# Performance work log

Hardware: AMD Instinct MI355X
Metric: run time of the kernel (lower is better)

## Reference

```python
import jax, jax.numpy as jnp
import numpy as np

NU, NI, D, C, V, E, L = 100000, 50000, 128, 5, 200000, 200000, 10


def setup_inputs() -> dict:
    key = jax.random.key(0)
    ks = jax.random.split(key, 16)
    s = lambda fan_in: 1.0 / np.sqrt(fan_in)
    return {
        "urf": jax.random.normal(ks[0], (NU, D), jnp.float32),
        "irf": jax.random.normal(ks[1], (NI, D), jnp.float32),
        "utf": jax.random.normal(ks[2], (NU, D), jnp.float32),
        "itf": jax.random.normal(ks[3], (NI, D), jnp.float32),
        "w1r": jax.random.normal(ks[4], (2 * D, D), jnp.float32) * s(2 * D),
        "w2r": jax.random.normal(ks[5], (D, D), jnp.float32) * s(D),
        "w1t": jax.random.normal(ks[6], (2 * D, D), jnp.float32) * s(2 * D),
        "w2t": jax.random.normal(ks[7], (D, D), jnp.float32) * s(D),
        "wp": jax.random.normal(ks[8], (D, C), jnp.float32) * s(D),
        "emb": jax.random.normal(ks[9], (V, D), jnp.float32),
        "src": jax.random.randint(ks[10], (E,), 0, NU, jnp.int32),
        "dst": jax.random.randint(ks[11], (E,), 0, NI, jnp.int32),
        "sentence_id": jax.random.randint(ks[12], (E, L), 0, V, jnp.int32),
        "neg_sid": jax.random.randint(ks[13], (E, L), 1, V, jnp.int32),
    }


def _review_feature(emb, sid):
    # masked mean-pool of sentence embeddings: [E, L] -> [E, D]
    length = (sid > 0).astype(jnp.float32).sum(axis=-1, keepdims=True) + 1e-9
    return emb[sid].sum(axis=-2) / length


def reference(urf, irf, utf, itf, w1r, w2r, w1t, w2t, wp, emb,
              src, dst, sentence_id, neg_sid):
    # edge-wise gather of src (user) / dst (item) features + concat  [E, 2D]
    rf = jnp.concatenate([urf[src], irf[dst]], axis=1)
    rh = jax.nn.relu(rf @ w1r) @ w2r                      # rating_linear  [E, D]
    pr = rh @ wp                                          # rating_predictor [E, C]
    tf = jnp.concatenate([utf[src], itf[dst]], axis=1)
    th = jax.nn.relu(tf @ w1t) @ w2t + rh                 # topic_linear + residual
    pos_review = _review_feature(emb, sentence_id)        # [E, D]
    neg_review = _review_feature(emb, neg_sid)            # [E, D]
    pos_score = (th * pos_review).sum(axis=1)             # [E]
    neg_score = (th * neg_review).sum(axis=1)
    loss = -jax.nn.log_sigmoid(pos_score - neg_score)     # -log(sigmoid(pos-neg))
    return pr, loss.mean(), loss.mean()
```

## Files before the change

### kernel.cpp

```cpp
#include <hip/hip_runtime.h>

#define NU_ 100000
#define NI_ 50000
#define D_  128
#define C_  5
#define V_  200000
#define E_  200000
#define L_  10

typedef __bf16 bf16x8 __attribute__((ext_vector_type(8)));
typedef unsigned short u16;
typedef u16 u16x8 __attribute__((ext_vector_type(8)));
typedef float f32x4 __attribute__((ext_vector_type(4)));

#define W1R_OFF 0
#define W2R_OFF 32768
#define W1T_OFF 49152
#define W2T_OFF 81920
#define WTOT    98304
#define EMB_BYTE_OFF (256 * 1024)
#define EMB_ELEMS    (V_ * D_)
#define TH_BYTE_OFF  (EMB_BYTE_OFF + EMB_ELEMS * 2)
#define TH_BYTES     ((size_t)E_ * D_ * 2)

__device__ __forceinline__ u16 f2bf(float x) {
    union { float f; unsigned int u; } v; v.f = x;
    unsigned int u = v.u;
    return (u16)((u + 0x7FFFu + ((u >> 16) & 1u)) >> 16);
}
__device__ __forceinline__ float bfhi(unsigned int u) {
    union { unsigned int u; float f; } v; v.u = u & 0xFFFF0000u; return v.f;
}
__device__ __forceinline__ float bflo(unsigned int u) {
    union { unsigned int u; float f; } v; v.u = u << 16; return v.f;
}

__global__ void prep_kernel(const float* __restrict__ w1r, const float* __restrict__ w2r,
                            const float* __restrict__ w1t, const float* __restrict__ w2t,
                            u16* __restrict__ wbuf, float* __restrict__ loss_acc) {
    int idx = blockIdx.x * blockDim.x + threadIdx.x;
    if (idx == 0) *loss_acc = 0.f;
    if (idx >= WTOT) return;
    const float* src; int base;
    if (idx < W2R_OFF)      { src = w1r; base = W1R_OFF; }
    else if (idx < W1T_OFF) { src = w2r; base = W2R_OFF; }
    else if (idx < W2T_OFF) { src = w1t; base = W1T_OFF; }
    else                    { src = w2t; base = W2T_OFF; }
    int local = idx - base;
    int j = local & 7;
    int g = local >> 3;
    int n = g & 127;
    int kq = g >> 7;
    wbuf[idx] = f2bf(src[(kq * 8 + j) * 128 + n]);
}

__global__ void cvt_kernel(const float* __restrict__ src, u16* __restrict__ dst, int n8) {
    int i = blockIdx.x * blockDim.x + threadIdx.x;
    if (i >= n8) return;
    float4 a = *(const float4*)(src + (size_t)i * 8);
    float4 b = *(const float4*)(src + (size_t)i * 8 + 4);
    u16x8 v;
    v[0] = f2bf(a.x); v[1] = f2bf(a.y); v[2] = f2bf(a.z); v[3] = f2bf(a.w);
    v[4] = f2bf(b.x); v[5] = f2bf(b.y); v[6] = f2bf(b.z); v[7] = f2bf(b.w);
    *(u16x8*)(dst + (size_t)i * 8) = v;
}

__device__ __forceinline__ void stage_half(const float* __restrict__ row, int lane, u16* buf) {
    int m = lane >> 2, q = lane & 3;
    const float* seg = row + q * 32;
#pragma unroll
    for (int i = 0; i < 4; i++) {
        float4 a = *(const float4*)(seg + i * 8);
        float4 b = *(const float4*)(seg + i * 8 + 4);
        u16x8 v;
        v[0] = f2bf(a.x); v[1] = f2bf(a.y); v[2] = f2bf(a.z); v[3] = f2bf(a.w);
        v[4] = f2bf(b.x); v[5] = f2bf(b.y); v[6] = f2bf(b.z); v[7] = f2bf(b.w);
        *(u16x8*)(buf + ((q * 4 + i) * 16 + m) * 8) = v;
    }
}

template <int KT>
__device__ __forceinline__ void gemm_tile(const u16* aLDS, const u16* __restrict__ Wg,
                                          int lq, int ln, f32x4 acc[8]) {
#pragma unroll
    for (int kt = 0; kt < KT; kt++) {
        bf16x8 af = *(const bf16x8*)(aLDS + ((kt * 4 + lq) * 16 + ln) * 8);
#pragma unroll
        for (int nt = 0; nt < 8; nt++) {
            bf16x8 bfv = *(const bf16x8*)(Wg + (size_t)((kt * 4 + lq) * 128 + nt * 16 + ln) * 8);
            acc[nt] = __builtin_amdgcn_mfma_f32_16x16x32_bf16(af, bfv, acc[nt], 0, 0, 0);
        }
    }
}

__device__ __forceinline__ void store_h_relu(const f32x4 acc[8], u16* buf, int lq, int ln) {
#pragma unroll
    for (int nt = 0; nt < 8; nt++)
#pragma unroll
        for (int reg = 0; reg < 4; reg++) {
            float h = fmaxf(acc[nt][reg], 0.f);
            int dcol = nt * 16 + ln;
            int r = lq * 4 + reg;
            buf[((dcol >> 3) * 16 + r) * 8 + (dcol & 7)] = f2bf(h);
        }
}

__device__ __forceinline__ void mlp(const float* __restrict__ uF, const float* __restrict__ iF,
                                    const int* __restrict__ srcI, const int* __restrict__ dstI,
                                    int ebase, int lane, int lq, int ln,
                                    const u16* __restrict__ w1, const u16* __restrict__ w2,
                                    u16* bufA, u16* bufB, f32x4 acc[8]) {
    int e = ebase + (lane >> 2);
    int su = srcI[e], sd = dstI[e];
    f32x4 h1[8];
#pragma unroll
    for (int nt = 0; nt < 8; nt++) h1[nt] = (f32x4){0.f, 0.f, 0.f, 0.f};

    stage_half(uF + (size_t)su * D_, lane, bufA);
    __syncthreads();
    gemm_tile<4>(bufA, w1, lq, ln, h1);
    __syncthreads();
    stage_half(iF + (size_t)sd * D_, lane, bufA);
    __syncthreads();
    gemm_tile<4>(bufA, w1 + 16384, lq, ln, h1);
    store_h_relu(h1, bufB, lq, ln);
    __syncthreads();
    gemm_tile<4>(bufB, w2, lq, ln, acc);
}

__device__ __forceinline__ float softplus_(float x) {
    return fmaxf(x, 0.f) + log1pf(expf(-fabsf(x)));
}


__global__ __launch_bounds__(256, 3) void mlp_kernel(
    const float* __restrict__ urf, const float* __restrict__ irf,
    const float* __restrict__ utf, const float* __restrict__ itf,
    const float* __restrict__ wp,
    const int* __restrict__ srcI, const int* __restrict__ dstI,
    const u16* __restrict__ wbuf, float* __restrict__ out,
    u16* __restrict__ thB) {
    __shared__ u16 smem[4 * 4096];
    const int tid = threadIdx.x;
    const int w = tid >> 6;
    const int lane = tid & 63;
    const int lq = lane >> 4;
    const int ln = lane & 15;
    u16* bufA = smem + w * 4096;
    u16* bufB = bufA + 2048;
    const int ebase = blockIdx.x * 64 + w * 16;

    f32x4 rh[8];
#pragma unroll
    for (int nt = 0; nt < 8; nt++) rh[nt] = (f32x4){0.f, 0.f, 0.f, 0.f};
    mlp(urf, irf, srcI, dstI, ebase, lane, lq, ln,
        wbuf + W1R_OFF, wbuf + W2R_OFF, bufA, bufB, rh);

    {
        float pp[4][5];
#pragma unroll
        for (int r = 0; r < 4; r++)
#pragma unroll
            for (int c = 0; c < 5; c++) pp[r][c] = 0.f;
#pragma unroll
        for (int nt = 0; nt < 8; nt++) {
            int d = nt * 16 + ln;
            float wpc[5];
#pragma unroll
            for (int c = 0; c < 5; c++) wpc[c] = wp[d * 5 + c];
#pragma unroll
            for (int reg = 0; reg < 4; reg++)
#pragma unroll
                for (int c = 0; c < 5; c++) pp[reg][c] += rh[nt][reg] * wpc[c];
        }
#pragma unroll
        for (int off = 1; off < 16; off <<= 1)
#pragma unroll
            for (int reg = 0; reg < 4; reg++)
#pragma unroll
                for (int c = 0; c < 5; c++)
                    pp[reg][c] += __shfl_xor(pp[reg][c], off, 64);
        if (ln == 0) {
#pragma unroll
            for (int reg = 0; reg < 4; reg++) {
                int e = ebase + lq * 4 + reg;
#pragma unroll
                for (int c = 0; c < 5; c++) out[(size_t)e * 5 + c] = pp[reg][c];
            }
        }
    }

    __syncthreads();
    f32x4 th[8];
#pragma unroll
    for (int nt = 0; nt < 8; nt++) th[nt] = rh[nt];
    mlp(utf, itf, srcI, dstI, ebase, lane, lq, ln,
        wbuf + W1T_OFF, wbuf + W2T_OFF, bufA, bufB, th);

    __syncthreads();
    float* thb = (float*)bufA;
#pragma unroll
    for (int nt = 0; nt < 8; nt++)
#pragma unroll
        for (int reg = 0; reg < 4; reg++)
            thb[(lq * 4 + reg) * 128 + nt * 16 + ln] = th[nt][reg];
    __syncthreads();

#pragma unroll
    for (int m = 0; m < 16; m++) {
        float2 ab = *(const float2*)(thb + m * 128 + lane * 2);
        unsigned pk = (unsigned)f2bf(ab.x) | ((unsigned)f2bf(ab.y) << 16);
        ((unsigned*)(thB + (size_t)(ebase + m) * D_))[lane] = pk;
    }
}

__global__ __launch_bounds__(256, 8) void review_kernel(
    const u16* __restrict__ thB, const u16* __restrict__ embB,
    const int* __restrict__ sidI, const int* __restrict__ nsidI,
    float* __restrict__ loss_acc) {
    __shared__ float red[4];
    const int tid = threadIdx.x;
    const int lane = tid & 63;
    const int gl = tid & 15;
    const int e = blockIdx.x * 16 + (tid >> 4);

    int ip = 0, in_ = 0;
    if (gl < L_) { ip = sidI[e * L_ + gl]; in_ = nsidI[e * L_ + gl]; }

    float th8[8];
    {
        union { u16x8 v; unsigned int u[4]; } tu;
        tu.v = *(const u16x8*)(thB + (size_t)e * D_ + gl * 8);
#pragma unroll
        for (int k = 0; k < 4; k++) {
            th8[2 * k]     = bflo(tu.u[k]);
            th8[2 * k + 1] = bfhi(tu.u[k]);
        }
    }

    float ps = 0.f, ns = 0.f;
    float pc = (gl < L_ && ip > 0) ? 1.f : 0.f;
    float nc = (gl < L_ && in_ > 0) ? 1.f : 0.f;

#pragma unroll
    for (int i = 0; i < L_; i++) {
        int s = __shfl(ip, i, 16);
        union { u16x8 v; unsigned int u[4]; } cv;
        cv.v = *(const u16x8*)(embB + (size_t)s * D_ + gl * 8);
        int t = __shfl(in_, i, 16);
        union { u16x8 v; unsigned int u[4]; } nv;
        nv.v = *(const u16x8*)(embB + (size_t)t * D_ + gl * 8);
#pragma unroll
        for (int k = 0; k < 4; k++) {
            ps = fmaf(th8[2 * k],     bflo(cv.u[k]), ps);
            ps = fmaf(th8[2 * k + 1], bfhi(cv.u[k]), ps);
        }
#pragma unroll
        for (int k = 0; k < 4; k++) {
            ns = fmaf(th8[2 * k],     bflo(nv.u[k]), ns);
            ns = fmaf(th8[2 * k + 1], bfhi(nv.u[k]), ns);
        }
    }

#pragma unroll
    for (int off = 1; off < 16; off <<= 1) {
        ps += __shfl_xor(ps, off, 64);
        ns += __shfl_xor(ns, off, 64);
        pc += __shfl_xor(pc, off, 64);
        nc += __shfl_xor(nc, off, 64);
    }
    float val = softplus_(ns / (nc + 1e-9f) - ps / (pc + 1e-9f));
    float wl = (gl == 0) ? val : 0.f;
    wl += __shfl_xor(wl, 16, 64);
    wl += __shfl_xor(wl, 32, 64);
    if (lane == 0) red[tid >> 6] = wl;
    __syncthreads();
    if (tid == 0) atomicAdd(loss_acc, red[0] + red[1] + red[2] + red[3]);
}

template <bool EB>
__global__ __launch_bounds__(256, 3) void fused_kernel(
    const float* __restrict__ urf, const float* __restrict__ irf,
    const float* __restrict__ utf, const float* __restrict__ itf,
    const float* __restrict__ wp, const float* __restrict__ emb,
    const u16* __restrict__ embB,
    const int* __restrict__ srcI, const int* __restrict__ dstI,
    const int* __restrict__ sidI, const int* __restrict__ nsidI,
    const u16* __restrict__ wbuf, float* __restrict__ loss_acc,
    float* __restrict__ out) {
    __shared__ u16 smem[4 * 4096];
    const int tid = threadIdx.x;
    const int w = tid >> 6;
    const int lane = tid & 63;
    const int lq = lane >> 4;
    const int ln = lane & 15;
    u16* bufA = smem + w * 4096;
    u16* bufB = bufA + 2048;
    const int ebase = blockIdx.x * 64 + w * 16;

    f32x4 rh[8];
#pragma unroll
    for (int nt = 0; nt < 8; nt++) rh[nt] = (f32x4){0.f, 0.f, 0.f, 0.f};
    mlp(urf, irf, srcI, dstI, ebase, lane, lq, ln,
        wbuf + W1R_OFF, wbuf + W2R_OFF, bufA, bufB, rh);

    {
        float pp[4][5];
#pragma unroll
        for (int r = 0; r < 4; r++)
#pragma unroll
            for (int c = 0; c < 5; c++) pp[r][c] = 0.f;
#pragma unroll
        for (int nt = 0; nt < 8; nt++) {
            int d = nt * 16 + ln;
            float wpc[5];
#pragma unroll
            for (int c = 0; c < 5; c++) wpc[c] = wp[d * 5 + c];
#pragma unroll
            for (int reg = 0; reg < 4; reg++)
#pragma unroll
                for (int c = 0; c < 5; c++) pp[reg][c] += rh[nt][reg] * wpc[c];
        }
#pragma unroll
        for (int off = 1; off < 16; off <<= 1)
#pragma unroll
            for (int reg = 0; reg < 4; reg++)
#pragma unroll
                for (int c = 0; c < 5; c++)
                    pp[reg][c] += __shfl_xor(pp[reg][c], off, 64);
        if (ln == 0) {
#pragma unroll
            for (int reg = 0; reg < 4; reg++) {
                int e = ebase + lq * 4 + reg;
#pragma unroll
                for (int c = 0; c < 5; c++) out[(size_t)e * 5 + c] = pp[reg][c];
            }
        }
    }

    __syncthreads();
    f32x4 th[8];
#pragma unroll
    for (int nt = 0; nt < 8; nt++) th[nt] = rh[nt];
    mlp(utf, itf, srcI, dstI, ebase, lane, lq, ln,
        wbuf + W1T_OFF, wbuf + W2T_OFF, bufA, bufB, th);

    __syncthreads();
    float* thb = (float*)bufA;
    if constexpr (EB) {
#pragma unroll
        for (int nt = 0; nt < 8; nt++)
#pragma unroll
            for (int reg = 0; reg < 4; reg++) {
                int col = nt * 16 + ln;
                thb[((lq * 4 + reg) * 16 + (col >> 3)) * 8 + (col & 7)] = th[nt][reg];
            }
    } else {
#pragma unroll
        for (int nt = 0; nt < 8; nt++)
#pragma unroll
            for (int reg = 0; reg < 4; reg++)
                thb[(lq * 4 + reg) * 128 + nt * 16 + ln] = th[nt][reg];
    }
    __syncthreads();

    float wave_loss = 0.f;
    if constexpr (EB) {
        const int g = lane >> 4, gl = lane & 15;
        for (int it = 0; it < 4; it++) {
            int m = it * 4 + g;
            int e = ebase + m;
            float th8[8];
            *(f32x4*)th8       = *(const f32x4*)(thb + (m * 16 + gl) * 8);
            *(f32x4*)(th8 + 4) = *(const f32x4*)(thb + (m * 16 + gl) * 8 + 4);
            float ps = 0.f, ns = 0.f;
            int pcnt = 0, ncnt = 0;
#pragma unroll
            for (int i = 0; i < L_; i++) {
                int s = sidI[e * L_ + i];
                pcnt += (s > 0) ? 1 : 0;
                union { u16x8 v; unsigned int u[4]; } cv;
                cv.v = *(const u16x8*)(embB + (size_t)s * D_ + gl * 8);
#pragma unroll
                for (int k = 0; k < 4; k++) {
                    ps = fmaf(th8[2 * k],     bflo(cv.u[k]), ps);
                    ps = fmaf(th8[2 * k + 1], bfhi(cv.u[k]), ps);
                }
            }
#pragma unroll
            for (int i = 0; i < L_; i++) {
                int s = nsidI[e * L_ + i];
                ncnt += (s > 0) ? 1 : 0;
                union { u16x8 v; unsigned int u[4]; } cv;
                cv.v = *(const u16x8*)(embB + (size_t)s * D_ + gl * 8);
#pragma unroll
                for (int k = 0; k < 4; k++) {
                    ns = fmaf(th8[2 * k],     bflo(cv.u[k]), ns);
                    ns = fmaf(th8[2 * k + 1], bfhi(cv.u[k]), ns);
                }
            }
#pragma unroll
            for (int off = 1; off < 16; off <<= 1) {
                ps += __shfl_xor(ps, off, 64);
                ns += __shfl_xor(ns, off, 64);
            }
            if (gl == 0) {
                ps /= ((float)pcnt + 1e-9f);
                ns /= ((float)ncnt + 1e-9f);
                wave_loss += softplus_(ns - ps);
            }
        }
        wave_loss += __shfl_xor(wave_loss, 16, 64);
        wave_loss += __shfl_xor(wave_loss, 32, 64);
    } else {
        const int h = lane >> 5, hl = lane & 31;
        for (int mp = 0; mp < 16; mp += 2) {
            int m = mp + h;
            int e = ebase + m;
            float4 t4 = *(const float4*)(thb + m * 128 + hl * 4);
            float ps = 0.f, ns = 0.f;
            int pcnt = 0, ncnt = 0;
#pragma unroll
            for (int i = 0; i < L_; i++) {
                int s = sidI[e * L_ + i];
                pcnt += (s > 0) ? 1 : 0;
                float4 ev = *(const float4*)(emb + (size_t)s * D_ + hl * 4);
                ps += t4.x * ev.x + t4.y * ev.y + t4.z * ev.z + t4.w * ev.w;
            }
#pragma unroll
            for (int i = 0; i < L_; i++) {
                int s = nsidI[e * L_ + i];
                ncnt += (s > 0) ? 1 : 0;
                float4 ev = *(const float4*)(emb + (size_t)s * D_ + hl * 4);
                ns += t4.x * ev.x + t4.y * ev.y + t4.z * ev.z + t4.w * ev.w;
            }
#pragma unroll
            for (int off = 1; off < 32; off <<= 1) {
                ps += __shfl_xor(ps, off, 64);
                ns += __shfl_xor(ns, off, 64);
            }
            if (hl == 0) {
                ps /= ((float)pcnt + 1e-9f);
                ns /= ((float)ncnt + 1e-9f);
                wave_loss += softplus_(ns - ps);
            }
        }
        wave_loss += __shfl_xor(wave_loss, 32, 64);
    }
    if (lane == 0) atomicAdd(loss_acc, wave_loss);
}

__global__ void finish_kernel(const float* __restrict__ loss_acc, float* __restrict__ out) {
    float v = loss_acc[0] * (1.0f / (float)E_);
    out[(size_t)E_ * C_]     = v;
    out[(size_t)E_ * C_ + 1] = v;
}

extern "C" void kernel_launch(void* const* d_in, const int* in_sizes, int n_in,
                              void* d_out, int out_size, void* d_ws, size_t ws_size,
                              hipStream_t stream) {
    const float* urf = (const float*)d_in[0];
    const float* irf = (const float*)d_in[1];
    const float* utf = (const float*)d_in[2];
    const float* itf = (const float*)d_in[3];
    const float* w1r = (const float*)d_in[4];
    const float* w2r = (const float*)d_in[5];
    const float* w1t = (const float*)d_in[6];
    const float* w2t = (const float*)d_in[7];
    const float* wp  = (const float*)d_in[8];
    const float* emb = (const float*)d_in[9];
    const int* srcI  = (const int*)d_in[10];
    const int* dstI  = (const int*)d_in[11];
    const int* sidI  = (const int*)d_in[12];
    const int* nsidI = (const int*)d_in[13];
    float* out = (float*)d_out;

    float* loss_acc = (float*)d_ws;
    u16* wbuf = (u16*)((char*)d_ws + 256);
    u16* embB = (u16*)((char*)d_ws + EMB_BYTE_OFF);
    u16* thB  = (u16*)((char*)d_ws + TH_BYTE_OFF);

    bool eb = ws_size >= (size_t)EMB_BYTE_OFF + (size_t)EMB_ELEMS * 2;
    bool tb = ws_size >= (size_t)TH_BYTE_OFF + TH_BYTES;

    prep_kernel<<<(WTOT + 255) / 256, 256, 0, stream>>>(w1r, w2r, w1t, w2t, wbuf, loss_acc);
    if (eb)
        cvt_kernel<<<(EMB_ELEMS / 8 + 255) / 256, 256, 0, stream>>>(emb, embB, EMB_ELEMS / 8);

    if (tb) {
        mlp_kernel<<<E_ / 64, 256, 0, stream>>>(
            urf, irf, utf, itf, wp, srcI, dstI, wbuf, out, thB);
        review_kernel<<<E_ / 16, 256, 0, stream>>>(
            thB, embB, sidI, nsidI, loss_acc);
    } else if (eb) {
        fused_kernel<true><<<E_ / 64, 256, 0, stream>>>(
            urf, irf, utf, itf, wp, emb, embB,
            srcI, dstI, sidI, nsidI, wbuf, loss_acc, out);
    } else {
        fused_kernel<false><<<E_ / 64, 256, 0, stream>>>(
            urf, irf, utf, itf, wp, emb, embB,
            srcI, dstI, sidI, nsidI, wbuf, loss_acc, out);
    }

    finish_kernel<<<1, 1, 0, stream>>>(loss_acc, out);
}
```

Measured before the change: 611.6 us.

## Quantize embedding table to FP8 and replace block barriers with per-wave LDS fences

The embedding table is now converted to an e4m3-style FP8 copy instead of bf16, which halves the bytes gathered in the review kernel and the bytes written by the conversion pass. The decode uses a shift-and-scale trick rather than hardware conversion. The MLP stages both the user and item halves into separate LDS buffers before the GEMMs, and replaces __syncthreads with wave-local lgkmcnt waits, since each wave owns its own LDS region. Costs: more LDS per block, larger quantization error in the review scores that may break tolerance, and the bf16-embedding fused fallback path is removed.

```diff
diff --git a/kernel.cpp b/kernel.cpp
--- a/kernel.cpp
+++ b/kernel.cpp
@@ -20,7 +20,7 @@
 #define WTOT    98304
 #define EMB_BYTE_OFF (256 * 1024)
 #define EMB_ELEMS    (V_ * D_)
-#define TH_BYTE_OFF  (EMB_BYTE_OFF + EMB_ELEMS * 2)
+#define TH_BYTE_OFF  (EMB_BYTE_OFF + EMB_ELEMS)
 #define TH_BYTES     ((size_t)E_ * D_ * 2)
 
 __device__ __forceinline__ u16 f2bf(float x) {
@@ -33,6 +33,29 @@
 }
 __device__ __forceinline__ float bflo(unsigned int u) {
     union { unsigned int u; float f; } v; v.u = u << 16; return v.f;
+}
+
+__device__ __forceinline__ unsigned f2fp8(float x) {
+    union { float f; unsigned u; } v; v.f = x;
+    unsigned s = (v.u >> 24) & 0x80u;
+    float ax = fabsf(x);
+    if (ax < 0.0078125f) return s;
+    if (ax < 0.015625f)  return s | 0x08u;
+    if (ax > 448.f)      return s | 0x7Eu;
+    unsigned u = v.u & 0x7FFFFFFFu;
+    unsigned r = u + 0x7FFFFu + ((u >> 20) & 1u);
+    unsigned c = (r >> 20) - 960u;
+    if (c > 0x7Eu) c = 0x7Eu;
+    return s | c;
+}
+__device__ __forceinline__ float fp8dec(unsigned b) {
+    unsigned t = ((b & 0x80u) << 24) | ((b & 0x7Fu) << 20);
+    union { unsigned u; float f; } v; v.u = t;
+    return v.f * 0x1.0p+120f;
+}
+
+__device__ __forceinline__ void lds_fence() {
+    asm volatile("s_waitcnt lgkmcnt(0)" ::: "memory");
 }
 
 __global__ void prep_kernel(const float* __restrict__ w1r, const float* __restrict__ w2r,
@@ -54,15 +77,15 @@
     wbuf[idx] = f2bf(src[(kq * 8 + j) * 128 + n]);
 }
 
-__global__ void cvt_kernel(const float* __restrict__ src, u16* __restrict__ dst, int n8) {
+__global__ void cvt8_kernel(const float* __restrict__ src, unsigned char* __restrict__ dst, int n8) {
     int i = blockIdx.x * blockDim.x + threadIdx.x;
     if (i >= n8) return;
     float4 a = *(const float4*)(src + (size_t)i * 8);
     float4 b = *(const float4*)(src + (size_t)i * 8 + 4);
-    u16x8 v;
-    v[0] = f2bf(a.x); v[1] = f2bf(a.y); v[2] = f2bf(a.z); v[3] = f2bf(a.w);
-    v[4] = f2bf(b.x); v[5] = f2bf(b.y); v[6] = f2bf(b.z); v[7] = f2bf(b.w);
-    *(u16x8*)(dst + (size_t)i * 8) = v;
+    uint2 v;
+    v.x = f2fp8(a.x) | (f2fp8(a.y) << 8) | (f2fp8(a.z) << 16) | (f2fp8(a.w) << 24);
+    v.y = f2fp8(b.x) | (f2fp8(b.y) << 8) | (f2fp8(b.z) << 16) | (f2fp8(b.w) << 24);
+    *(uint2*)(dst + (size_t)i * 8) = v;
 }
 
 __device__ __forceinline__ void stage_half(const float* __restrict__ row, int lane, u16* buf) {
@@ -105,26 +128,20 @@
         }
 }
 
-__device__ __forceinline__ void mlp(const float* __restrict__ uF, const float* __restrict__ iF,
-                                    const int* __restrict__ srcI, const int* __restrict__ dstI,
-                                    int ebase, int lane, int lq, int ln,
-                                    const u16* __restrict__ w1, const u16* __restrict__ w2,
-                                    u16* bufA, u16* bufB, f32x4 acc[8]) {
-    int e = ebase + (lane >> 2);
-    int su = srcI[e], sd = dstI[e];
+__device__ __forceinline__ void mlp2(const float* __restrict__ uRow, const float* __restrict__ iRow,
+                                     int lane, int lq, int ln,
+                                     const u16* __restrict__ w1, const u16* __restrict__ w2,
+                                     u16* bufA, u16* bufC, u16* bufB, f32x4 acc[8]) {
     f32x4 h1[8];
 #pragma unroll
     for (int nt = 0; nt < 8; nt++) h1[nt] = (f32x4){0.f, 0.f, 0.f, 0.f};
-
-    stage_half(uF + (size_t)su * D_, lane, bufA);
-    __syncthreads();
+    stage_half(uRow, lane, bufA);
+    stage_half(iRow, lane, bufC);
+    lds_fence();
     gemm_tile<4>(bufA, w1, lq, ln, h1);
-    __syncthreads();
-    stage_half(iF + (size_t)sd * D_, lane, bufA);
-    __syncthreads();
-    gemm_tile<4>(bufA, w1 + 16384, lq, ln, h1);
+    gemm_tile<4>(bufC, w1 + 16384, lq, ln, h1);
     store_h_relu(h1, bufB, lq, ln);
-    __syncthreads();
+    lds_fence();
     gemm_tile<4>(bufB, w2, lq, ln, acc);
 }
 
@@ -140,21 +157,25 @@
     const int* __restrict__ srcI, const int* __restrict__ dstI,
     const u16* __restrict__ wbuf, float* __restrict__ out,
     u16* __restrict__ thB) {
-    __shared__ u16 smem[4 * 4096];
+    __shared__ u16 smem[4 * 6144];
     const int tid = threadIdx.x;
     const int w = tid >> 6;
     const int lane = tid & 63;
     const int lq = lane >> 4;
     const int ln = lane & 15;
-    u16* bufA = smem + w * 4096;
-    u16* bufB = bufA + 2048;
+    u16* bufA = smem + w * 6144;
+    u16* bufC = bufA + 2048;
+    u16* bufB = bufA + 4096;
     const int ebase = blockIdx.x * 64 + w * 16;
 
+    const int e0 = ebase + (lane >> 2);
+    const int su = srcI[e0], sd = dstI[e0];
+
     f32x4 rh[8];
 #pragma unroll
     for (int nt = 0; nt < 8; nt++) rh[nt] = (f32x4){0.f, 0.f, 0.f, 0.f};
-    mlp(urf, irf, srcI, dstI, ebase, lane, lq, ln,
-        wbuf + W1R_OFF, wbuf + W2R_OFF, bufA, bufB, rh);
+    mlp2(urf + (size_t)su * D_, irf + (size_t)sd * D_, lane, lq, ln,
+         wbuf + W1R_OFF, wbuf + W2R_OFF, bufA, bufC, bufB, rh);
 
     {
         float pp[4][5];
@@ -190,21 +211,19 @@
         }
     }
 
-    __syncthreads();
     f32x4 th[8];
 #pragma unroll
     for (int nt = 0; nt < 8; nt++) th[nt] = rh[nt];
-    mlp(utf, itf, srcI, dstI, ebase, lane, lq, ln,
-        wbuf + W1T_OFF, wbuf + W2T_OFF, bufA, bufB, th);
-
-    __syncthreads();
+    mlp2(utf + (size_t)su * D_, itf + (size_t)sd * D_, lane, lq, ln,
+         wbuf + W1T_OFF, wbuf + W2T_OFF, bufA, bufC, bufB, th);
+
     float* thb = (float*)bufA;
 #pragma unroll
     for (int nt = 0; nt < 8; nt++)
 #pragma unroll
         for (int reg = 0; reg < 4; reg++)
             thb[(lq * 4 + reg) * 128 + nt * 16 + ln] = th[nt][reg];
-    __syncthreads();
+    lds_fence();
 
 #pragma unroll
     for (int m = 0; m < 16; m++) {
@@ -215,7 +234,7 @@
 }
 
 __global__ __launch_bounds__(256, 8) void review_kernel(
-    const u16* __restrict__ thB, const u16* __restrict__ embB,
+    const u16* __restrict__ thB, const unsigned char* __restrict__ embF8,
     const int* __restrict__ sidI, const int* __restrict__ nsidI,
     float* __restrict__ loss_acc) {
     __shared__ float red[4];
@@ -245,20 +264,18 @@
 #pragma unroll
     for (int i = 0; i < L_; i++) {
         int s = __shfl(ip, i, 16);
-        union { u16x8 v; unsigned int u[4]; } cv;
-        cv.v = *(const u16x8*)(embB + (size_t)s * D_ + gl * 8);
+        uint2 cv = *(const uint2*)(embF8 + (size_t)s * D_ + gl * 8);
         int t = __shfl(in_, i, 16);
-        union { u16x8 v; unsigned int u[4]; } nv;
-        nv.v = *(const u16x8*)(embB + (size_t)t * D_ + gl * 8);
-#pragma unroll
-        for (int k = 0; k < 4; k++) {
-            ps = fmaf(th8[2 * k],     bflo(cv.u[k]), ps);
-            ps = fmaf(th8[2 * k + 1], bfhi(cv.u[k]), ps);
-        }
-#pragma unroll
-        for (int k = 0; k < 4; k++) {
-            ns = fmaf(th8[2 * k],     bflo(nv.u[k]), ns);
-            ns = fmaf(th8[2 * k + 1], bfhi(nv.u[k]), ns);
+        uint2 nv = *(const uint2*)(embF8 + (size_t)t * D_ + gl * 8);
+#pragma unroll
+        for (int j = 0; j < 4; j++) {
+            ps = fmaf(th8[j],     fp8dec((cv.x >> (8 * j)) & 0xFFu), ps);
+            ps = fmaf(th8[4 + j], fp8dec((cv.y >> (8 * j)) & 0xFFu), ps);
+        }
+#pragma unroll
+        for (int j = 0; j < 4; j++) {
+            ns = fmaf(th8[j],     fp8dec((nv.x >> (8 * j)) & 0xFFu), ns);
+            ns = fmaf(th8[4 + j], fp8dec((nv.y >> (8 * j)) & 0xFFu), ns);
         }
     }
 
@@ -278,31 +295,32 @@
     if (tid == 0) atomicAdd(loss_acc, red[0] + red[1] + red[2] + red[3]);
 }
 
-template <bool EB>
 __global__ __launch_bounds__(256, 3) void fused_kernel(
     const float* __restrict__ urf, const float* __restrict__ irf,
     const float* __restrict__ utf, const float* __restrict__ itf,
     const float* __restrict__ wp, const float* __restrict__ emb,
-    const u16* __restrict__ embB,
     const int* __restrict__ srcI, const int* __restrict__ dstI,
     const int* __restrict__ sidI, const int* __restrict__ nsidI,
     const u16* __restrict__ wbuf, float* __restrict__ loss_acc,
     float* __restrict__ out) {
-    __shared__ u16 smem[4 * 4096];
+    __shared__ u16 smem[4 * 6144];
     const int tid = threadIdx.x;
     const int w = tid >> 6;
     const int lane = tid & 63;
     const int lq = lane >> 4;
     const int ln = lane & 15;
-    u16* bufA = smem + w * 4096;
-    u16* bufB = bufA + 2048;
+    u16* bufA = smem + w * 6144;
+    u16* bufC = bufA + 2048;
+    u16* bufB = bufA + 4096;
     const int ebase = blockIdx.x * 64 + w * 16;
+    const int e0 = ebase + (lane >> 2);
+    const int su = srcI[e0], sd = dstI[e0];
 
     f32x4 rh[8];
 #pragma unroll
     for (int nt = 0; nt < 8; nt++) rh[nt] = (f32x4){0.f, 0.f, 0.f, 0.f};
-    mlp(urf, irf, srcI, dstI, ebase, lane, lq, ln,
-        wbuf + W1R_OFF, wbuf + W2R_OFF, bufA, bufB, rh);
+    mlp2(urf + (size_t)su * D_, irf + (size_t)sd * D_, lane, lq, ln,
+         wbuf + W1R_OFF, wbuf + W2R_OFF, bufA, bufC, bufB, rh);
 
     {
         float pp[4][5];
@@ -338,81 +356,22 @@
         }
     }
 
-    __syncthreads();
     f32x4 th[8];
 #pragma unroll
     for (int nt = 0; nt < 8; nt++) th[nt] = rh[nt];
-    mlp(utf, itf, srcI, dstI, ebase, lane, lq, ln,
-        wbuf + W1T_OFF, wbuf + W2T_OFF, bufA, bufB, th);
-
-    __syncthreads();
+    mlp2(utf + (size_t)su * D_, itf + (size_t)sd * D_, lane, lq, ln,
+         wbuf + W1T_OFF, wbuf + W2T_OFF, bufA, bufC, bufB, th);
+
     float* thb = (float*)bufA;
-    if constexpr (EB) {
-#pragma unroll
-        for (int nt = 0; nt < 8; nt++)
-#pragma unroll
-            for (int reg = 0; reg < 4; reg++) {
-                int col = nt * 16 + ln;
-                thb[((lq * 4 + reg) * 16 + (col >> 3)) * 8 + (col & 7)] = th[nt][reg];
-            }
-    } else {
-#pragma unroll
-        for (int nt = 0; nt < 8; nt++)
-#pragma unroll
-            for (int reg = 0; reg < 4; reg++)
-                thb[(lq * 4 + reg) * 128 + nt * 16 + ln] = th[nt][reg];
-    }
-    __syncthreads();
+#pragma unroll
+    for (int nt = 0; nt < 8; nt++)
+#pragma unroll
+        for (int reg = 0; reg < 4; reg++)
+            thb[(lq * 4 + reg) * 128 + nt * 16 + ln] = th[nt][reg];
+    lds_fence();
 
     float wave_loss = 0.f;
-    if constexpr (EB) {
-        const int g = lane >> 4, gl = lane & 15;
-        for (int it = 0; it < 4; it++) {
-            int m = it * 4 + g;
-            int e = ebase + m;
-            float th8[8];
-            *(f32x4*)th8       = *(const f32x4*)(thb + (m * 16 + gl) * 8);
-            *(f32x4*)(th8 + 4) = *(const f32x4*)(thb + (m * 16 + gl) * 8 + 4);
-            float ps = 0.f, ns = 0.f;
-            int pcnt = 0, ncnt = 0;
-#pragma unroll
-            for (int i = 0; i < L_; i++) {
-                int s = sidI[e * L_ + i];
-                pcnt += (s > 0) ? 1 : 0;
-                union { u16x8 v; unsigned int u[4]; } cv;
-                cv.v = *(const u16x8*)(embB + (size_t)s * D_ + gl * 8);
-#pragma unroll
-                for (int k = 0; k < 4; k++) {
-                    ps = fmaf(th8[2 * k],     bflo(cv.u[k]), ps);
-                    ps = fmaf(th8[2 * k + 1], bfhi(cv.u[k]), ps);
-                }
-            }
-#pragma unroll
-            for (int i = 0; i < L_; i++) {
-                int s = nsidI[e * L_ + i];
-                ncnt += (s > 0) ? 1 : 0;
-                union { u16x8 v; unsigned int u[4]; } cv;
-                cv.v = *(const u16x8*)(embB + (size_t)s * D_ + gl * 8);
-#pragma unroll
-                for (int k = 0; k < 4; k++) {
-                    ns = fmaf(th8[2 * k],     bflo(cv.u[k]), ns);
-                    ns = fmaf(th8[2 * k + 1], bfhi(cv.u[k]), ns);
-                }
-            }
-#pragma unroll
-            for (int off = 1; off < 16; off <<= 1) {
-                ps += __shfl_xor(ps, off, 64);
-                ns += __shfl_xor(ns, off, 64);
-            }
-            if (gl == 0) {
-                ps /= ((float)pcnt + 1e-9f);
-                ns /= ((float)ncnt + 1e-9f);
-                wave_loss += softplus_(ns - ps);
-            }
-        }
-        wave_loss += __shfl_xor(wave_loss, 16, 64);
-        wave_loss += __shfl_xor(wave_loss, 32, 64);
-    } else {
+    {
         const int h = lane >> 5, hl = lane & 31;
         for (int mp = 0; mp < 16; mp += 2) {
             int m = mp + h;
@@ -477,29 +436,23 @@
 
     float* loss_acc = (float*)d_ws;
     u16* wbuf = (u16*)((char*)d_ws + 256);
-    u16* embB = (u16*)((char*)d_ws + EMB_BYTE_OFF);
+    unsigned char* embF8 = (unsigned char*)d_ws + EMB_BYTE_OFF;
     u16* thB  = (u16*)((char*)d_ws + TH_BYTE_OFF);
 
-    bool eb = ws_size >= (size_t)EMB_BYTE_OFF + (size_t)EMB_ELEMS * 2;
     bool tb = ws_size >= (size_t)TH_BYTE_OFF + TH_BYTES;
 
     prep_kernel<<<(WTOT + 255) / 256, 256, 0, stream>>>(w1r, w2r, w1t, w2t, wbuf, loss_acc);
-    if (eb)
-        cvt_kernel<<<(EMB_ELEMS / 8 + 255) / 256, 256, 0, stream>>>(emb, embB, EMB_ELEMS / 8);
 
     if (tb) {
+        cvt8_kernel<<<(EMB_ELEMS / 8 + 255) / 256, 256, 0, stream>>>(emb, embF8, EMB_ELEMS / 8);
         mlp_kernel<<<E_ / 64, 256, 0, stream>>>(
             urf, irf, utf, itf, wp, srcI, dstI, wbuf, out, thB);
         review_kernel<<<E_ / 16, 256, 0, stream>>>(
-            thB, embB, sidI, nsidI, loss_acc);
-    } else if (eb) {
-        fused_kernel<true><<<E_ / 64, 256, 0, stream>>>(
-            urf, irf, utf, itf, wp, emb, embB,
+            thB, embF8, sidI, nsidI, loss_acc);
+    } else {
+        fused_kernel<<<E_ / 64, 256, 0, stream>>>(
+            urf, irf, utf, itf, wp, emb,
             srcI, dstI, sidI, nsidI, wbuf, loss_acc, out);
-    } else {
-        fused_kernel<false><<<E_ / 64, 256, 0, stream>>>(
-            urf, irf, utf, itf, wp, emb, embB,
-            srcI, dstI, sidI, nsidI, wbuf, loss_acc, out);
     }
 
     finish_kernel<<<1, 1, 0, stream>>>(loss_acc, out);
```

After: 600.5 us. Within noise of the previous version (-1.8%).
